# Performance work log

Hardware: AMD Instinct MI355X
Metric: run time of the kernel (lower is better)

Reference implementation:

```python
import jax, jax.numpy as jnp
import numpy as np

R = 2          # candidate_radius
TEMP = 0.1     # temperature
MIN_E = 3
MAX_E = 8      # max_edges_per_node
EPS = 1e-6


def _neighbors(H, W, r):
    # grid neighbor indices (N,K) and relative positions (K,2), clamped at borders
    ys, xs = np.meshgrid(np.arange(H), np.arange(W), indexing='ij')
    idx_grid = ys * W + xs
    nbrs, rel = [], []
    for dy in range(-r, r + 1):
        for dx in range(-r, r + 1):
            if dy == 0 and dx == 0:
                continue
            ny = np.clip(ys + dy, 0, H - 1)
            nx = np.clip(xs + dx, 0, W - 1)
            nbrs.append(idx_grid[ny, nx].ravel())
            rel.append([dx / r, dy / r])
    return jnp.asarray(np.stack(nbrs, 1)), jnp.asarray(np.array(rel, np.float32))


def setup_inputs() -> dict:
    key = jax.random.key(0)
    ks = jax.random.split(key, 12)
    B, C, H, W = 2, 64, 128, 128
    hid = 64
    ein = 2 * C + 2  # edge scorer input dim
    s = 0.05
    return {
        'x':  jax.random.normal(ks[0], (B, C, H, W), jnp.float32),
        'W1': jax.random.normal(ks[1], (hid, ein), jnp.float32) * s,
        'b1': jnp.zeros((hid,), jnp.float32),
        'W2': jax.random.normal(ks[2], (hid // 2, hid), jnp.float32) * s,
        'b2': jnp.zeros((hid // 2,), jnp.float32),
        'W3': jax.random.normal(ks[3], (1, hid // 2), jnp.float32) * s,
        'b3': jnp.zeros((1,), jnp.float32),
        'thr': jnp.asarray(0.0, jnp.float32),
        'Wm': jax.random.normal(ks[4], (C, C), jnp.float32) * s,
        'bm': jnp.zeros((C,), jnp.float32),
        'Wo': jax.random.normal(ks[5], (C, C), jnp.float32) * s,
        'bo': jnp.zeros((C,), jnp.float32),
    }


def reference(x, W1, b1, W2, b2, W3, b3, thr, Wm, bm, Wo, bo):
    B, C, H, W = x.shape
    N = H * W
    nbr, rel = _neighbors(H, W, R)          # (N,K), (K,2)
    K = nbr.shape[1]

    nodes = x.transpose(0, 2, 3, 1).reshape(B, N, C)   # (B,N,C)
    h_tgt = jnp.take(nodes, nbr, axis=1)               # (B,N,K,C) gather neighbors

    # edge scorer layer1: split W1 over [h_src | h_tgt | rel_pos] to avoid (B,N,K,2C+2) concat
    z_src = nodes @ W1[:, :C].T                        # (B,N,hid)
    z_tgt = h_tgt @ W1[:, C:2 * C].T                   # (B,N,K,hid)
    z_pos = rel @ W1[:, 2 * C:].T                      # (K,hid)
    h1 = jax.nn.relu(z_src[:, :, None, :] + z_tgt + z_pos[None, None] + b1)
    h2 = jax.nn.relu(h1 @ W2.T + b2)
    edge_scores = jax.nn.sigmoid((h2 @ W3.T + b3)[..., 0])   # (B,N,K)

    thr_v = jax.nn.sigmoid(thr)
    keep_prob = jax.nn.sigmoid((edge_scores - thr_v) / TEMP)
    mask_thr = edge_scores >= thr_v
    counts = mask_thr.sum(axis=2)                       # (B,N)

    def topk_mask(k):
        _, idx = jax.lax.top_k(edge_scores, k)          # (B,N,k)
        return jax.nn.one_hot(idx, K, dtype=jnp.float32).sum(-2) > 0

    m_max = topk_mask(min(MAX_E, K))
    m_min = topk_mask(min(MIN_E, K))
    use_max = (counts > MAX_E)[..., None]
    use_min = (counts < MIN_E)[..., None]
    use_t = ~use_max & ~use_min
    final_mask = (use_max & m_max) | (use_min & m_min) | (use_t & mask_thr)

    msgs = jax.nn.relu(h_tgt @ Wm.T + bm)               # (B,N,K,C)
    w = (edge_scores * keep_prob * final_mask.astype(edge_scores.dtype))[..., None]
    agg = (msgs * w).sum(axis=2) / (w.sum(axis=2) + EPS)  # (B,N,C)

    out = nodes + agg @ Wo.T + bo
    return out.reshape(B, H, W, C).transpose(0, 3, 1, 2)
```

## Files before the change

kernel.cpp:

```cpp
#include <hip/hip_runtime.h>
#include <hip/hip_bf16.h>
#include <math.h>

#define NNODES 16384
#define KE 24

typedef float f32x4 __attribute__((ext_vector_type(4)));
typedef unsigned u32x4 __attribute__((ext_vector_type(4)));
typedef __fp16 half2_t __attribute__((ext_vector_type(2)));
typedef _Float16 half8_t __attribute__((ext_vector_type(8)));

union fragcast { u32x4 u; half8_t h; half2_t h2[4]; };

__global__ __launch_bounds__(256) void precompute_k(
    const float* __restrict__ x, const float* __restrict__ W1,
    const float* __restrict__ Wm, const float* __restrict__ b1,
    const float* __restrict__ bm,
    float* __restrict__ zsrc, float* __restrict__ ztgt, float* __restrict__ msg,
    float* __restrict__ zpos)
{
    __shared__ fragcast fragA[64 * 17];
    __shared__ float otL[4][16 * 68];

    const int t = threadIdx.x;
    const int l = t & 63;
    const int lcol = l & 15;
    const int lgrp = l >> 4;
    const int w = t >> 6;
    const int mat = blockIdx.x >> 8;
    const int tile = blockIdx.x & 255;
    const int n0g = tile * 128;
    const int b = n0g >> 14;
    const int nl0 = n0g & (NNODES - 1);

    if (blockIdx.x == 0) {
        for (int idx = t; idx < KE * 64; idx += 256) {
            int k = idx >> 6, h = idx & 63;
            int kk = k + (k >= 12 ? 1 : 0);
            int q5 = (kk * 52) >> 8;
            int dy = q5 - 2, dx = kk - 5 * q5 - 2;
            zpos[idx] = W1[h * 130 + 128] * (dx * 0.5f)
                      + W1[h * 130 + 129] * (dy * 0.5f);
        }
    }

    {
        const int mt = w;
        const int h = mt * 16 + lcol;
        const float* wrow = (mat == 0) ? (W1 + (size_t)h * 130)
                          : (mat == 1) ? (W1 + (size_t)h * 130 + 64)
                                       : (Wm + (size_t)h * 64);
        #pragma unroll
        for (int kt = 0; kt < 2; ++kt) {
            const float* wr = wrow + kt * 32 + lgrp * 8;
            fragcast fh, fl;
            #pragma unroll
            for (int d = 0; d < 4; ++d) {
                float e0 = wr[2 * d] * 64.f;
                float e1 = wr[2 * d + 1] * 64.f;
                half2_t hh = __builtin_amdgcn_cvt_pkrtz(e0, e1);
                fh.h2[d] = hh;
                fl.h2[d] = __builtin_amdgcn_cvt_pkrtz(e0 - (float)hh[0],
                                                      e1 - (float)hh[1]);
            }
            fragA[l * 17 + mt * 4 + kt * 2 + 0] = fh;
            fragA[l * 17 + mt * 4 + kt * 2 + 1] = fl;
        }
    }
    __syncthreads();

    float bv[4][4];
    #pragma unroll
    for (int mt = 0; mt < 4; ++mt)
        #pragma unroll
        for (int q = 0; q < 4; ++q) {
            int h = mt * 16 + lgrp * 4 + q;
            bv[mt][q] = (mat == 0) ? b1[h] : (mat == 2) ? bm[h] : 0.f;
        }

    const fragcast* fa = &fragA[l * 17];
    const float* xb = x + (size_t)b * 64 * NNODES + nl0;
    float* dst = (mat == 0) ? zsrc : (mat == 1) ? ztgt : msg;
    float* ot = &otL[w][0];

    #pragma unroll 1
    for (int nt = 0; nt < 2; ++nt) {
        const int nloc = w * 32 + nt * 16;

        fragcast Bh[2], Bl[2];
        #pragma unroll
        for (int kt = 0; kt < 2; ++kt) {
            const float* xc = xb + (size_t)(kt * 32 + lgrp * 8) * NNODES + nloc + lcol;
            float xv[8];
            #pragma unroll
            for (int i = 0; i < 8; ++i) xv[i] = xc[(size_t)i * NNODES];
            #pragma unroll
            for (int d = 0; d < 4; ++d) {
                half2_t hh = __builtin_amdgcn_cvt_pkrtz(xv[2 * d], xv[2 * d + 1]);
                Bh[kt].h2[d] = hh;
                Bl[kt].h2[d] = __builtin_amdgcn_cvt_pkrtz(xv[2 * d] - (float)hh[0],
                                                          xv[2 * d + 1] - (float)hh[1]);
            }
        }

        #pragma unroll
        for (int mt = 0; mt < 4; ++mt) {
            f32x4 acc = {0.f, 0.f, 0.f, 0.f};
            #pragma unroll
            for (int kt = 0; kt < 2; ++kt) {
                fragcast Ah = fa[mt * 4 + kt * 2 + 0];
                fragcast Al = fa[mt * 4 + kt * 2 + 1];
                acc = __builtin_amdgcn_mfma_f32_16x16x32_f16(Ah.h, Bh[kt].h, acc, 0, 0, 0);
                acc = __builtin_amdgcn_mfma_f32_16x16x32_f16(Al.h, Bh[kt].h, acc, 0, 0, 0);
                acc = __builtin_amdgcn_mfma_f32_16x16x32_f16(Ah.h, Bl[kt].h, acc, 0, 0, 0);
            }
            #pragma unroll
            for (int q = 0; q < 4; ++q) {
                float v = fmaf(acc[q], 0.015625f, bv[mt][q]);
                if (mat == 2) v = fmaxf(v, 0.f);
                ot[lcol * 68 + mt * 16 + lgrp * 4 + q] = v;
            }
        }

        {
            int nn = l >> 2, qt = l & 3;
            float* gout = dst + (size_t)(n0g + nloc + nn) * 64 + qt * 16;
            #pragma unroll
            for (int j = 0; j < 4; ++j) {
                f32x4 vv = *(const f32x4*)&ot[nn * 68 + qt * 16 + j * 4];
                *(float4*)(gout + j * 4) = make_float4(vv[0], vv[1], vv[2], vv[3]);
            }
        }
    }
}

__global__ __launch_bounds__(256, 3) void score_k(
    const float* __restrict__ zsrc, const float* __restrict__ ztgt,
    const float* __restrict__ zpos, const float* __restrict__ W2,
    const float* __restrict__ b2, const float* __restrict__ W3,
    const float* __restrict__ b3, float* __restrict__ scores)
{
    __shared__ fragcast fraglds[64 * 13];

    const int t = threadIdx.x;
    const int l = t & 63;
    const int lcol = l & 15;
    const int lgrp = l >> 4;
    const int w = t >> 6;
    const int wave = blockIdx.x * 4 + w;

    {
        const int jt = w >> 1, kt = w & 1;
        fragcast fh, fl;
        const float* wr = W2 + (size_t)(jt * 16 + lcol) * 64 + kt * 32 + lgrp * 8;
        #pragma unroll
        for (int d = 0; d < 4; ++d) {
            float e0 = wr[2 * d] * 64.f;
            float e1 = wr[2 * d + 1] * 64.f;
            half2_t hh = __builtin_amdgcn_cvt_pkrtz(e0, e1);
            float r0 = e0 - (float)hh[0];
            float r1 = e1 - (float)hh[1];
            fh.h2[d] = hh;
            fl.h2[d] = __builtin_amdgcn_cvt_pkrtz(r0, r1);
        }
        fraglds[l * 13 + 0 + jt * 2 + kt] = fh;
        fraglds[l * 13 + 4 + jt * 2 + kt] = fl;
    }
    __syncthreads();

    const fragcast* fb = &fraglds[l * 13];
    const f32x4 b2l0 = *(const f32x4*)(b2 + lgrp * 4);
    const f32x4 b2l1 = *(const f32x4*)(b2 + 16 + lgrp * 4);
    const f32x4 w3l0 = *(const f32x4*)(W3 + lgrp * 4);
    const f32x4 w3l1 = *(const f32x4*)(W3 + 16 + lgrp * 4);
    const float b3s = b3[0];

    const int node0 = wave * 2;

    int kArr[3];
    float4 zsv[3][4], ztv[3][4];
    #pragma unroll
    for (int Mt = 0; Mt < 3; ++Mt) {
        const int ke = Mt * 16 + lcol;
        const int nsel = (ke >= 24) ? 1 : 0;
        const int node = node0 + nsel;
        const int k = ke - 24 * nsel;
        const int bb = node >> 14;
        const int nl = node & (NNODES - 1);
        const int yy = nl >> 7, xx = nl & 127;
        const int kk = k + (k >= 12 ? 1 : 0);
        const int q5 = (kk * 52) >> 8;
        const int dy = q5 - 2, dx = kk - 5 * q5 - 2;
        const int ny = min(max(yy + dy, 0), 127);
        const int nx = min(max(xx + dx, 0), 127);
        const int nbn = (bb << 14) + (ny << 7) + nx;
        kArr[Mt] = k;
        const float* zs = zsrc + (size_t)node * 64 + lgrp * 8;
        const float* zt = ztgt + (size_t)nbn * 64 + lgrp * 8;
        zsv[Mt][0] = *(const float4*)(zs);
        zsv[Mt][1] = *(const float4*)(zs + 4);
        zsv[Mt][2] = *(const float4*)(zs + 32);
        zsv[Mt][3] = *(const float4*)(zs + 36);
        ztv[Mt][0] = *(const float4*)(zt);
        ztv[Mt][1] = *(const float4*)(zt + 4);
        ztv[Mt][2] = *(const float4*)(zt + 32);
        ztv[Mt][3] = *(const float4*)(zt + 36);
    }

    #pragma unroll
    for (int Mt = 0; Mt < 3; ++Mt) {
        const float* zp = zpos + kArr[Mt] * 64 + lgrp * 8;

        f32x4 ac0A = {0.f,0.f,0.f,0.f}, ac0B = {0.f,0.f,0.f,0.f};
        f32x4 ac1A = {0.f,0.f,0.f,0.f}, ac1B = {0.f,0.f,0.f,0.f};

        #pragma unroll
        for (int kt = 0; kt < 2; ++kt) {
            float4 a0 = zsv[Mt][2 * kt], a1 = zsv[Mt][2 * kt + 1];
            float4 t0 = ztv[Mt][2 * kt], t1 = ztv[Mt][2 * kt + 1];
            float4 p0 = *(const float4*)(zp + kt * 32);
            float4 p1 = *(const float4*)(zp + kt * 32 + 4);
            float v[8];
            v[0] = fmaxf(a0.x + t0.x + p0.x, 0.f);
            v[1] = fmaxf(a0.y + t0.y + p0.y, 0.f);
            v[2] = fmaxf(a0.z + t0.z + p0.z, 0.f);
            v[3] = fmaxf(a0.w + t0.w + p0.w, 0.f);
            v[4] = fmaxf(a1.x + t1.x + p1.x, 0.f);
            v[5] = fmaxf(a1.y + t1.y + p1.y, 0.f);
            v[6] = fmaxf(a1.z + t1.z + p1.z, 0.f);
            v[7] = fmaxf(a1.w + t1.w + p1.w, 0.f);

            fragcast Bh, Bl;
            #pragma unroll
            for (int d = 0; d < 4; ++d) {
                float e0 = v[2 * d], e1 = v[2 * d + 1];
                half2_t hh = __builtin_amdgcn_cvt_pkrtz(e0, e1);
                float r0 = e0 - (float)hh[0];
                float r1 = e1 - (float)hh[1];
                Bh.h2[d] = hh;
                Bl.h2[d] = __builtin_amdgcn_cvt_pkrtz(r0, r1);
            }

            ac0A = __builtin_amdgcn_mfma_f32_16x16x32_f16(fb[0 + kt].h, Bh.h, ac0A, 0, 0, 0);
            ac1A = __builtin_amdgcn_mfma_f32_16x16x32_f16(fb[2 + kt].h, Bh.h, ac1A, 0, 0, 0);
            ac0B = __builtin_amdgcn_mfma_f32_16x16x32_f16(fb[4 + kt].h, Bh.h, ac0B, 0, 0, 0);
            ac1B = __builtin_amdgcn_mfma_f32_16x16x32_f16(fb[6 + kt].h, Bh.h, ac1B, 0, 0, 0);
            ac0B = __builtin_amdgcn_mfma_f32_16x16x32_f16(fb[0 + kt].h, Bl.h, ac0B, 0, 0, 0);
            ac1B = __builtin_amdgcn_mfma_f32_16x16x32_f16(fb[2 + kt].h, Bl.h, ac1B, 0, 0, 0);
        }

        const f32x4 s0 = ac0A + ac0B;
        const f32x4 s1 = ac1A + ac1B;
        float sacc = 0.f;
        #pragma unroll
        for (int q = 0; q < 4; ++q) {
            sacc = fmaf(fmaxf(fmaf(s0[q], 0.015625f, b2l0[q]), 0.f), w3l0[q], sacc);
            sacc = fmaf(fmaxf(fmaf(s1[q], 0.015625f, b2l1[q]), 0.f), w3l1[q], sacc);
        }
        sacc += __shfl_xor(sacc, 16);
        sacc += __shfl_xor(sacc, 32);
        float sig = 1.f / (1.f + expf(-(sacc + b3s)));
        if (l < 16)
            scores[(size_t)node0 * 24 + Mt * 16 + l] = sig;
    }
}

__global__ __launch_bounds__(256) void agg_k(
    const float* __restrict__ x, const float* __restrict__ scores,
    const float* __restrict__ msg, const float* __restrict__ Wo,
    const float* __restrict__ bo, const float* __restrict__ thrp,
    float* __restrict__ out)
{
    __shared__ float sc[768];
    __shared__ float wl[768];
    __shared__ float sumw[32];
    __shared__ float aggL[32][64];
    __shared__ float ot[64][33];

    const int t = threadIdx.x;
    const int n0 = blockIdx.x * 32;
    const int b = n0 >> 14;
    const int nl0 = n0 & (NNODES - 1);
    const float thr_v = 1.f / (1.f + expf(-thrp[0]));

    #pragma unroll
    for (int rep = 0; rep < 3; ++rep)
        sc[rep * 256 + t] = scores[(size_t)n0 * 24 + rep * 256 + t];
    __syncthreads();

    #pragma unroll
    for (int rep = 0; rep < 3; ++rep) {
        int e = rep * 256 + t;
        int nl = (int)(((unsigned)(e >> 3) * 171u) >> 9);
        int k = e - nl * 24;
        float s_e = sc[e];
        int rank = 0, cnt = 0;
        #pragma unroll
        for (int j = 0; j < 24; ++j) {
            float sj = sc[nl * 24 + j];
            rank += (sj > s_e || (sj == s_e && j < k)) ? 1 : 0;
            cnt  += (sj >= thr_v) ? 1 : 0;
        }
        bool mask = (cnt > 8) ? (rank < 8)
                  : ((cnt < 3) ? (rank < 3) : (s_e >= thr_v));
        float keep = 1.f / (1.f + expf(-(s_e - thr_v) * 10.f));
        wl[e] = mask ? s_e * keep : 0.f;
    }
    __syncthreads();

    if (t < 32) {
        float s = 0.f;
        #pragma unroll
        for (int k = 0; k < 24; ++k) s += wl[t * 24 + k];
        sumw[t] = s + 1e-6f;
    }
    __syncthreads();

    const int lane = t & 63;
    const int g4 = t >> 6;

    #pragma unroll
    for (int it = 0; it < 8; ++it) {
        int nl = g4 + it * 4;
        int nn = nl0 + nl;
        int yy = nn >> 7, xx = nn & 127;
        float acc = 0.f;
        #pragma unroll
        for (int k = 0; k < 24; ++k) {
            int kk = k + (k >= 12 ? 1 : 0);
            int q5 = (kk * 52) >> 8;
            int dy = q5 - 2, dx = kk - 5 * q5 - 2;
            int ny = min(max(yy + dy, 0), 127);
            int nx = min(max(xx + dx, 0), 127);
            int nb = (b << 14) + (ny << 7) + nx;
            acc = fmaf(wl[nl * 24 + k], msg[(size_t)nb * 64 + lane], acc);
        }
        aggL[nl][lane] = acc / sumw[nl];
    }

    float4 wo[16];
    #pragma unroll
    for (int c4 = 0; c4 < 16; ++c4) wo[c4] = ((const float4*)Wo)[lane * 16 + c4];
    __syncthreads();

    #pragma unroll
    for (int it = 0; it < 8; ++it) {
        int nl = g4 + it * 4;
        const float4* ar = (const float4*)aggL[nl];
        float a0 = 0.f, a1 = 0.f, a2 = 0.f, a3 = 0.f;
        #pragma unroll
        for (int c4 = 0; c4 < 16; ++c4) {
            float4 wv = wo[c4];
            float4 av = ar[c4];
            a0 = fmaf(av.x, wv.x, a0);
            a1 = fmaf(av.y, wv.y, a1);
            a2 = fmaf(av.z, wv.z, a2);
            a3 = fmaf(av.w, wv.w, a3);
        }
        float v = (a0 + a1) + (a2 + a3) + bo[lane]
                + x[(size_t)b * 64 * NNODES + (size_t)lane * NNODES + nl0 + nl];
        ot[lane][nl] = v;
    }
    __syncthreads();

    #pragma unroll
    for (int rep = 0; rep < 2; ++rep) {
        int idx = rep * 256 + t;
        int o = idx >> 3, p = idx & 7;
        float4 v = make_float4(ot[o][4 * p + 0], ot[o][4 * p + 1],
                               ot[o][4 * p + 2], ot[o][4 * p + 3]);
        *(float4*)(out + (size_t)b * 64 * NNODES + (size_t)o * NNODES + nl0 + 4 * p) = v;
    }
}

extern "C" void kernel_launch(void* const* d_in, const int* in_sizes, int n_in,
                              void* d_out, int out_size, void* d_ws, size_t ws_size,
                              hipStream_t stream)
{
    const float* x   = (const float*)d_in[0];
    const float* W1  = (const float*)d_in[1];
    const float* b1  = (const float*)d_in[2];
    const float* W2  = (const float*)d_in[3];
    const float* b2  = (const float*)d_in[4];
    const float* W3  = (const float*)d_in[5];
    const float* b3  = (const float*)d_in[6];
    const float* thr = (const float*)d_in[7];
    const float* Wm  = (const float*)d_in[8];
    const float* bm  = (const float*)d_in[9];
    const float* Wo  = (const float*)d_in[10];
    const float* bo  = (const float*)d_in[11];
    float* out = (float*)d_out;
    float* ws  = (float*)d_ws;

    float* zsrc   = ws;
    float* ztgt   = ws + 2097152;
    float* msg    = ws + 4194304;
    float* scores = ws + 6291456;
    float* zpos   = ws + 7077888;

    hipLaunchKernelGGL(precompute_k, dim3(768), dim3(256), 0, stream,
                       x, W1, Wm, b1, bm, zsrc, ztgt, msg, zpos);
    hipLaunchKernelGGL(score_k, dim3(4096), dim3(256), 0, stream,
                       zsrc, ztgt, zpos, W2, b2, W3, b3, scores);
    hipLaunchKernelGGL(agg_k, dim3(1024), dim3(256), 0, stream,
                       x, scores, msg, Wo, bo, thr, out);
}
```

Baseline: 102.5 us.

## Remap score kernel so each wave handles 16 nodes for one neighbor offset

Each wave of the edge-scoring kernel used to cover 2 nodes and all 24 neighbor offsets in three MFMA tiles. It now covers 16 consecutive nodes for a single offset, so the zpos row is uniform per wave and the neighbor gathers follow a contiguous shifted stencil. The grid grows to 12288 blocks and launch bounds rise to 4 blocks per CU to raise occupancy. In exchange, each block rebuilds the W2 fragments in LDS three times as often, and score writes now stride by 24 floats instead of being contiguous.

```diff
diff --git a/kernel.cpp b/kernel.cpp
--- a/kernel.cpp
+++ b/kernel.cpp
@@ -134,7 +134,7 @@
     }
 }
 
-__global__ __launch_bounds__(256, 3) void score_k(
+__global__ __launch_bounds__(256, 4) void score_k(
     const float* __restrict__ zsrc, const float* __restrict__ ztgt,
     const float* __restrict__ zpos, const float* __restrict__ W2,
     const float* __restrict__ b2, const float* __restrict__ W3,
@@ -147,7 +147,11 @@
     const int lcol = l & 15;
     const int lgrp = l >> 4;
     const int w = t >> 6;
-    const int wave = blockIdx.x * 4 + w;
+
+    const int bid = blockIdx.x;
+    const int ns = (int)((((unsigned long long)(bid >> 3)) * 0xAAAAAAABull) >> 33);
+    const int k  = bid - ns * 24;
+    const int node0 = ns * 64 + w * 16;
 
     {
         const int jt = w >> 1, kt = w & 1;
@@ -175,94 +179,80 @@
     const f32x4 w3l1 = *(const f32x4*)(W3 + 16 + lgrp * 4);
     const float b3s = b3[0];
 
-    const int node0 = wave * 2;
-
-    int kArr[3];
-    float4 zsv[3][4], ztv[3][4];
-    #pragma unroll
-    for (int Mt = 0; Mt < 3; ++Mt) {
-        const int ke = Mt * 16 + lcol;
-        const int nsel = (ke >= 24) ? 1 : 0;
-        const int node = node0 + nsel;
-        const int k = ke - 24 * nsel;
-        const int bb = node >> 14;
-        const int nl = node & (NNODES - 1);
-        const int yy = nl >> 7, xx = nl & 127;
-        const int kk = k + (k >= 12 ? 1 : 0);
-        const int q5 = (kk * 52) >> 8;
-        const int dy = q5 - 2, dx = kk - 5 * q5 - 2;
-        const int ny = min(max(yy + dy, 0), 127);
-        const int nx = min(max(xx + dx, 0), 127);
-        const int nbn = (bb << 14) + (ny << 7) + nx;
-        kArr[Mt] = k;
-        const float* zs = zsrc + (size_t)node * 64 + lgrp * 8;
-        const float* zt = ztgt + (size_t)nbn * 64 + lgrp * 8;
-        zsv[Mt][0] = *(const float4*)(zs);
-        zsv[Mt][1] = *(const float4*)(zs + 4);
-        zsv[Mt][2] = *(const float4*)(zs + 32);
-        zsv[Mt][3] = *(const float4*)(zs + 36);
-        ztv[Mt][0] = *(const float4*)(zt);
-        ztv[Mt][1] = *(const float4*)(zt + 4);
-        ztv[Mt][2] = *(const float4*)(zt + 32);
-        ztv[Mt][3] = *(const float4*)(zt + 36);
-    }
-
-    #pragma unroll
-    for (int Mt = 0; Mt < 3; ++Mt) {
-        const float* zp = zpos + kArr[Mt] * 64 + lgrp * 8;
-
-        f32x4 ac0A = {0.f,0.f,0.f,0.f}, ac0B = {0.f,0.f,0.f,0.f};
-        f32x4 ac1A = {0.f,0.f,0.f,0.f}, ac1B = {0.f,0.f,0.f,0.f};
-
-        #pragma unroll
-        for (int kt = 0; kt < 2; ++kt) {
-            float4 a0 = zsv[Mt][2 * kt], a1 = zsv[Mt][2 * kt + 1];
-            float4 t0 = ztv[Mt][2 * kt], t1 = ztv[Mt][2 * kt + 1];
-            float4 p0 = *(const float4*)(zp + kt * 32);
-            float4 p1 = *(const float4*)(zp + kt * 32 + 4);
-            float v[8];
-            v[0] = fmaxf(a0.x + t0.x + p0.x, 0.f);
-            v[1] = fmaxf(a0.y + t0.y + p0.y, 0.f);
-            v[2] = fmaxf(a0.z + t0.z + p0.z, 0.f);
-            v[3] = fmaxf(a0.w + t0.w + p0.w, 0.f);
-            v[4] = fmaxf(a1.x + t1.x + p1.x, 0.f);
-            v[5] = fmaxf(a1.y + t1.y + p1.y, 0.f);
-            v[6] = fmaxf(a1.z + t1.z + p1.z, 0.f);
-            v[7] = fmaxf(a1.w + t1.w + p1.w, 0.f);
-
-            fragcast Bh, Bl;
-            #pragma unroll
-            for (int d = 0; d < 4; ++d) {
-                float e0 = v[2 * d], e1 = v[2 * d + 1];
-                half2_t hh = __builtin_amdgcn_cvt_pkrtz(e0, e1);
-                float r0 = e0 - (float)hh[0];
-                float r1 = e1 - (float)hh[1];
-                Bh.h2[d] = hh;
-                Bl.h2[d] = __builtin_amdgcn_cvt_pkrtz(r0, r1);
-            }
-
-            ac0A = __builtin_amdgcn_mfma_f32_16x16x32_f16(fb[0 + kt].h, Bh.h, ac0A, 0, 0, 0);
-            ac1A = __builtin_amdgcn_mfma_f32_16x16x32_f16(fb[2 + kt].h, Bh.h, ac1A, 0, 0, 0);
-            ac0B = __builtin_amdgcn_mfma_f32_16x16x32_f16(fb[4 + kt].h, Bh.h, ac0B, 0, 0, 0);
-            ac1B = __builtin_amdgcn_mfma_f32_16x16x32_f16(fb[6 + kt].h, Bh.h, ac1B, 0, 0, 0);
-            ac0B = __builtin_amdgcn_mfma_f32_16x16x32_f16(fb[0 + kt].h, Bl.h, ac0B, 0, 0, 0);
-            ac1B = __builtin_amdgcn_mfma_f32_16x16x32_f16(fb[2 + kt].h, Bl.h, ac1B, 0, 0, 0);
-        }
-
-        const f32x4 s0 = ac0A + ac0B;
-        const f32x4 s1 = ac1A + ac1B;
-        float sacc = 0.f;
-        #pragma unroll
-        for (int q = 0; q < 4; ++q) {
-            sacc = fmaf(fmaxf(fmaf(s0[q], 0.015625f, b2l0[q]), 0.f), w3l0[q], sacc);
-            sacc = fmaf(fmaxf(fmaf(s1[q], 0.015625f, b2l1[q]), 0.f), w3l1[q], sacc);
-        }
-        sacc += __shfl_xor(sacc, 16);
-        sacc += __shfl_xor(sacc, 32);
-        float sig = 1.f / (1.f + expf(-(sacc + b3s)));
-        if (l < 16)
-            scores[(size_t)node0 * 24 + Mt * 16 + l] = sig;
-    }
+    const int kk = k + (k >= 12 ? 1 : 0);
+    const int q5 = (kk * 52) >> 8;
+    const int dy = q5 - 2, dx = kk - 5 * q5 - 2;
+
+    const int node = node0 + lcol;
+    const int bb = node >> 14;
+    const int nl = node & (NNODES - 1);
+    const int yy = nl >> 7, xx = nl & 127;
+    const int ny = min(max(yy + dy, 0), 127);
+    const int nx = min(max(xx + dx, 0), 127);
+    const int nbn = (bb << 14) + (ny << 7) + nx;
+
+    const float* zs = zsrc + (size_t)node * 64 + lgrp * 8;
+    const float* zt = ztgt + (size_t)nbn * 64 + lgrp * 8;
+    const float* zp = zpos + k * 64 + lgrp * 8;
+
+    float4 zsv[4], ztv[4], zpv[4];
+    zsv[0] = *(const float4*)(zs);      zsv[1] = *(const float4*)(zs + 4);
+    zsv[2] = *(const float4*)(zs + 32); zsv[3] = *(const float4*)(zs + 36);
+    ztv[0] = *(const float4*)(zt);      ztv[1] = *(const float4*)(zt + 4);
+    ztv[2] = *(const float4*)(zt + 32); ztv[3] = *(const float4*)(zt + 36);
+    zpv[0] = *(const float4*)(zp);      zpv[1] = *(const float4*)(zp + 4);
+    zpv[2] = *(const float4*)(zp + 32); zpv[3] = *(const float4*)(zp + 36);
+
+    f32x4 ac0A = {0.f,0.f,0.f,0.f}, ac0B = {0.f,0.f,0.f,0.f};
+    f32x4 ac1A = {0.f,0.f,0.f,0.f}, ac1B = {0.f,0.f,0.f,0.f};
+
+    #pragma unroll
+    for (int kt = 0; kt < 2; ++kt) {
+        float4 a0 = zsv[2 * kt], a1 = zsv[2 * kt + 1];
+        float4 t0 = ztv[2 * kt], t1 = ztv[2 * kt + 1];
+        float4 p0 = zpv[2 * kt], p1 = zpv[2 * kt + 1];
+        float v[8];
+        v[0] = fmaxf(a0.x + t0.x + p0.x, 0.f);
+        v[1] = fmaxf(a0.y + t0.y + p0.y, 0.f);
+        v[2] = fmaxf(a0.z + t0.z + p0.z, 0.f);
+        v[3] = fmaxf(a0.w + t0.w + p0.w, 0.f);
+        v[4] = fmaxf(a1.x + t1.x + p1.x, 0.f);
+        v[5] = fmaxf(a1.y + t1.y + p1.y, 0.f);
+        v[6] = fmaxf(a1.z + t1.z + p1.z, 0.f);
+        v[7] = fmaxf(a1.w + t1.w + p1.w, 0.f);
+
+        fragcast Bh, Bl;
+        #pragma unroll
+        for (int d = 0; d < 4; ++d) {
+            float e0 = v[2 * d], e1 = v[2 * d + 1];
+            half2_t hh = __builtin_amdgcn_cvt_pkrtz(e0, e1);
+            float r0 = e0 - (float)hh[0];
+            float r1 = e1 - (float)hh[1];
+            Bh.h2[d] = hh;
+            Bl.h2[d] = __builtin_amdgcn_cvt_pkrtz(r0, r1);
+        }
+
+        ac0A = __builtin_amdgcn_mfma_f32_16x16x32_f16(fb[0 + kt].h, Bh.h, ac0A, 0, 0, 0);
+        ac1A = __builtin_amdgcn_mfma_f32_16x16x32_f16(fb[2 + kt].h, Bh.h, ac1A, 0, 0, 0);
+        ac0B = __builtin_amdgcn_mfma_f32_16x16x32_f16(fb[4 + kt].h, Bh.h, ac0B, 0, 0, 0);
+        ac1B = __builtin_amdgcn_mfma_f32_16x16x32_f16(fb[6 + kt].h, Bh.h, ac1B, 0, 0, 0);
+        ac0B = __builtin_amdgcn_mfma_f32_16x16x32_f16(fb[0 + kt].h, Bl.h, ac0B, 0, 0, 0);
+        ac1B = __builtin_amdgcn_mfma_f32_16x16x32_f16(fb[2 + kt].h, Bl.h, ac1B, 0, 0, 0);
+    }
+
+    const f32x4 s0 = ac0A + ac0B;
+    const f32x4 s1 = ac1A + ac1B;
+    float sacc = 0.f;
+    #pragma unroll
+    for (int q = 0; q < 4; ++q) {
+        sacc = fmaf(fmaxf(fmaf(s0[q], 0.015625f, b2l0[q]), 0.f), w3l0[q], sacc);
+        sacc = fmaf(fmaxf(fmaf(s1[q], 0.015625f, b2l1[q]), 0.f), w3l1[q], sacc);
+    }
+    sacc += __shfl_xor(sacc, 16);
+    sacc += __shfl_xor(sacc, 32);
+    float sig = 1.f / (1.f + expf(-(sacc + b3s)));
+    if (l < 16)
+        scores[(size_t)(node0 + l) * 24 + k] = sig;
 }
 
 __global__ __launch_bounds__(256) void agg_k(
@@ -400,7 +390,7 @@
 
     hipLaunchKernelGGL(precompute_k, dim3(768), dim3(256), 0, stream,
                        x, W1, Wm, b1, bm, zsrc, ztgt, msg, zpos);
-    hipLaunchKernelGGL(score_k, dim3(4096), dim3(256), 0, stream,
+    hipLaunchKernelGGL(score_k, dim3(12288), dim3(256), 0, stream,
                        zsrc, ztgt, zpos, W2, b2, W3, b3, scores);
     hipLaunchKernelGGL(agg_k, dim3(1024), dim3(256), 0, stream,
                        x, scores, msg, Wo, bo, thr, out);
```

After: 115.3 us. 12.5% more time.
